# Kernel optimization log

Measured on AMD Instinct MI355X. Metric: run time of the kernel, lower is better.

## Reference

```python
import jax, jax.numpy as jnp
import numpy as np
import math

NUM_HEADS = 16
NUM_KV_HEADS = 4
HEAD_DIM = 128
HIDDEN = 2048
ROPE_BASE = 10000.0


def setup_inputs() -> dict:
    key = jax.random.key(0)
    ks = jax.random.split(key, 6)
    B, S = 1, 4096
    hidden_states = jax.random.normal(ks[0], (B, S, HIDDEN), dtype=jnp.float32)
    attention_mask = jnp.ones((B, S), dtype=jnp.int32)
    position_ids = jnp.broadcast_to(jnp.arange(S, dtype=jnp.int32)[None, :], (B, S))
    sc = 1.0 / math.sqrt(HIDDEN)
    wq = jax.random.normal(ks[1], (HIDDEN, NUM_HEADS * HEAD_DIM), dtype=jnp.float32) * sc
    wk = jax.random.normal(ks[2], (HIDDEN, NUM_KV_HEADS * HEAD_DIM), dtype=jnp.float32) * sc
    wv = jax.random.normal(ks[3], (HIDDEN, NUM_KV_HEADS * HEAD_DIM), dtype=jnp.float32) * sc
    wo = jax.random.normal(ks[4], (NUM_HEADS * HEAD_DIM, HIDDEN), dtype=jnp.float32) * sc
    return {"hidden_states": hidden_states, "attention_mask": attention_mask,
            "position_ids": position_ids, "wq": wq, "wk": wk, "wv": wv, "wo": wo}


def _rotate_half(x):
    x1, x2 = jnp.split(x, 2, axis=-1)
    return jnp.concatenate((-x2, x1), axis=-1)


def _rope_tables(seq_len, dtype):
    inv_freq = 1.0 / (ROPE_BASE ** (jnp.arange(0, HEAD_DIM, 2, dtype=jnp.float32) / HEAD_DIM))
    t = jnp.arange(seq_len, dtype=jnp.float32)
    freqs = jnp.outer(t, inv_freq)                       # [S, hd/2]
    emb = jnp.concatenate((freqs, freqs), axis=-1)       # [S, hd]
    return jnp.cos(emb).astype(dtype), jnp.sin(emb).astype(dtype)


def reference(hidden_states, attention_mask, position_ids, wq, wk, wv, wo):
    B, S, _ = hidden_states.shape
    dtype = hidden_states.dtype
    # projections -> [B, H, S, hd]
    q = (hidden_states @ wq).reshape(B, S, NUM_HEADS, HEAD_DIM).transpose(0, 2, 1, 3)
    k = (hidden_states @ wk).reshape(B, S, NUM_KV_HEADS, HEAD_DIM).transpose(0, 2, 1, 3)
    v = (hidden_states @ wv).reshape(B, S, NUM_KV_HEADS, HEAD_DIM).transpose(0, 2, 1, 3)
    # RoPE
    cos_t, sin_t = _rope_tables(S, dtype)
    cos = cos_t[position_ids][:, None]                   # [B,1,S,hd]
    sin = sin_t[position_ids][:, None]
    q = q * cos + _rotate_half(q) * sin
    k = k * cos + _rotate_half(k) * sin
    # GQA repeat
    n_rep = NUM_HEADS // NUM_KV_HEADS
    k = jnp.repeat(k, n_rep, axis=1)
    v = jnp.repeat(v, n_rep, axis=1)
    # scores + causal mask + padding mask
    scores = jnp.einsum('bhqd,bhkd->bhqk', q, k) / math.sqrt(HEAD_DIM)
    neg = jnp.finfo(scores.dtype).min
    causal = jnp.triu(jnp.full((S, S), neg, dtype=scores.dtype), k=1)
    scores = scores + causal[None, None]
    pad = (1.0 - attention_mask.astype(scores.dtype))[:, None, None, :] * neg
    scores = scores + pad
    attn = jax.nn.softmax(scores.astype(jnp.float32), axis=-1).astype(dtype)
    out = jnp.einsum('bhqk,bhkd->bhqd', attn, v)
    out = out.transpose(0, 2, 1, 3).reshape(B, S, NUM_HEADS * HEAD_DIM)
    return out @ wo
```

## Files before the change

### kernel.cpp

```cpp
#include <hip/hip_runtime.h>
#include <cstdint>
#include <cstddef>

typedef unsigned short ushort_t;
typedef short    bf16x8 __attribute__((ext_vector_type(8)));
typedef float    f32x4  __attribute__((ext_vector_type(4)));
typedef uint4    __attribute__((may_alias)) uint4_a;
typedef ushort4  __attribute__((may_alias)) ushort4_a;
typedef float4   __attribute__((may_alias)) float4_a;
typedef float2   __attribute__((may_alias)) float2_a;
typedef unsigned __attribute__((may_alias)) uint_a;

constexpr int SEQ = 4096, HID = 2048, NHEADS = 16, NKVH = 4, HDIM = 128;
constexpr int QD  = NHEADS * HDIM;
constexpr int KVD = NKVH * HDIM;
constexpr int KVL = 2 * KVD;
constexpr int NPART = 56;

static __device__ __forceinline__ float bf2f(ushort_t u) {
    return __uint_as_float(((unsigned)u) << 16);
}
static __device__ __forceinline__ ushort_t f2bf(float f) {
    unsigned x = __float_as_uint(f);
    unsigned r = x + 0x7FFFu + ((x >> 16) & 1u);
    return (ushort_t)(r >> 16);
}
static __device__ __forceinline__ unsigned pack2(float lo, float hi) {
    return (unsigned)f2bf(lo) | ((unsigned)f2bf(hi) << 16);
}
static __device__ __forceinline__ unsigned cvt_pk(float lo, float hi) {
    unsigned r;
    asm("v_cvt_pk_bf16_f32 %0, %1, %2" : "=v"(r) : "v"(lo), "v"(hi));
    return r;
}

static __device__ __forceinline__ void gld16(const ushort_t* g, ushort_t* l) {
    __builtin_amdgcn_global_load_lds(
        (const __attribute__((address_space(1))) unsigned*)g,
        (__attribute__((address_space(3))) unsigned*)l, 16, 0, 0);
}

__global__ __launch_bounds__(256) void cast_f32_bf16(
    const float* __restrict__ in, ushort_t* __restrict__ out, int n)
{
    int i = (blockIdx.x * 256 + threadIdx.x) * 8;
    if (i >= n) return;
    float4 a = *(const float4_a*)(in + i);
    float4 b = *(const float4_a*)(in + i + 4);
    uint4 o;
    o.x = pack2(a.x, a.y); o.y = pack2(a.z, a.w);
    o.z = pack2(b.x, b.y); o.w = pack2(b.z, b.w);
    *(uint4_a*)(out + i) = o;
}

__global__ __launch_bounds__(256) void transpose_cast(
    const float* __restrict__ W, ushort_t* __restrict__ WT, int K, int N)
{
    __shared__ float tl[32][36];
    const int k0 = blockIdx.x * 32, n0 = blockIdx.y * 32;
    const int t  = threadIdx.x;
    {
        int i = t >> 3, jb = (t & 7) * 4;
        *(float4_a*)&tl[i][jb] = *(const float4_a*)(W + (size_t)(k0 + i) * N + n0 + jb);
    }
    __syncthreads();
    {
        int n = t >> 3, kb = (t & 7) * 4;
        ushort4 o;
        o.x = f2bf(tl[kb + 0][n]); o.y = f2bf(tl[kb + 1][n]);
        o.z = f2bf(tl[kb + 2][n]); o.w = f2bf(tl[kb + 3][n]);
        *(ushort4_a*)(WT + (size_t)(n0 + n) * K + k0 + kb) = o;
    }
}

__global__ __launch_bounds__(256) void gemm_mfma(
    const ushort_t* __restrict__ A, int lda,
    const ushort_t* __restrict__ Bt, int ldb,
    void* __restrict__ C1, int ld1, void* __restrict__ C2, int ld2,
    int split, int N, int K, int out_f32)
{
    __shared__ ushort_t as[128 * 32];
    __shared__ ushort_t bs[128 * 32];

    const int t    = threadIdx.x;
    const int mb   = blockIdx.y * 128, nb = blockIdx.x * 128;
    const int w    = t >> 6, lane = t & 63, quad = lane >> 4, l15 = lane & 15;
    const int wm   = (w >> 1) * 64, wn = (w & 1) * 64;

    const int dr_row = lane >> 2, dr_c = lane & 3;
    const int rA0 = w * 16 + dr_row, rA1 = 64 + w * 16 + dr_row;
    const ushort_t* a0p = A  + (size_t)(mb + rA0) * lda + (dr_c ^ (rA0 & 3)) * 8;
    const ushort_t* a1p = A  + (size_t)(mb + rA1) * lda + (dr_c ^ (rA1 & 3)) * 8;
    const ushort_t* b0p = Bt + (size_t)(nb + rA0) * ldb + (dr_c ^ (rA0 & 3)) * 8;
    const ushort_t* b1p = Bt + (size_t)(nb + rA1) * ldb + (dr_c ^ (rA1 & 3)) * 8;
    ushort_t* asb0 = &as[(w) * 512];        ushort_t* asb1 = &as[(4 + w) * 512];
    ushort_t* bsb0 = &bs[(w) * 512];        ushort_t* bsb1 = &bs[(4 + w) * 512];

    f32x4 acc[4][4];
#pragma unroll
    for (int i = 0; i < 4; i++)
#pragma unroll
        for (int j = 0; j < 4; j++) acc[i][j] = (f32x4)0.f;

    const int chunk = quad ^ (l15 & 3);

    for (int kb = 0; kb < K; kb += 32) {
        __syncthreads();
        gld16(a0p + kb, asb0);
        gld16(a1p + kb, asb1);
        gld16(b0p + kb, bsb0);
        gld16(b1p + kb, bsb1);
        __syncthreads();

        bf16x8 af[4], bf[4];
#pragma unroll
        for (int mt = 0; mt < 4; mt++)
            af[mt] = *(const bf16x8*)&as[(wm + mt * 16 + l15) * 32 + chunk * 8];
#pragma unroll
        for (int nt = 0; nt < 4; nt++)
            bf[nt] = *(const bf16x8*)&bs[(wn + nt * 16 + l15) * 32 + chunk * 8];
#pragma unroll
        for (int mt = 0; mt < 4; mt++)
#pragma unroll
            for (int nt = 0; nt < 4; nt++)
                acc[mt][nt] = __builtin_amdgcn_mfma_f32_16x16x32_bf16(
                    af[mt], bf[nt], acc[mt][nt], 0, 0, 0);
    }

#pragma unroll
    for (int mt = 0; mt < 4; mt++)
#pragma unroll
        for (int nt = 0; nt < 4; nt++) {
            int colg = nb + wn + nt * 16 + l15;
#pragma unroll
            for (int r = 0; r < 4; r++) {
                int row = mb + wm + mt * 16 + quad * 4 + r;
                float v = acc[mt][nt][r];
                if (out_f32)            ((float*)C1)[(size_t)row * ld1 + colg] = v;
                else if (colg < split)  ((ushort_t*)C1)[(size_t)row * ld1 + colg] = f2bf(v);
                else                    ((ushort_t*)C2)[(size_t)row * ld2 + colg - split] = f2bf(v);
            }
        }
}

__global__ __launch_bounds__(256) void rope_bf16(
    ushort_t* __restrict__ buf, int ld, int nh, const int* __restrict__ pos_ids)
{
    int idx  = blockIdx.x * 256 + threadIdx.x;
    int i    = idx & 63;
    int rem  = idx >> 6;
    int head = rem % nh;
    int s    = rem / nh;
    if (s >= SEQ) return;

    float pos = (float)pos_ids[s];
    float ang = pos * __expf(-(float)i * 0.14391156831212787f);
    float c, sn;
    sincosf(ang, &sn, &c);

    ushort_t* p = buf + (size_t)s * ld + head * HDIM;
    float x0 = bf2f(p[i]);
    float x1 = bf2f(p[i + 64]);
    p[i]      = f2bf(x0 * c - x1 * sn);
    p[i + 64] = f2bf(x1 * c + x0 * sn);
}

__global__ __launch_bounds__(512, 4) void flash_mfma(
    const ushort_t* Q, const ushort_t* __restrict__ KV,
    const int* __restrict__ amask, ushort_t* O,
    ushort_t* __restrict__ Opart, float2* __restrict__ ML)
{
    __shared__ ushort_t ks[64][136];
    __shared__ ushort_t vt[128][72];
    __shared__ float    bias[64];

    const int t = threadIdx.x, w = t >> 6, lane = t & 63;
    const int quad = lane >> 4, l15 = lane & 15;
    const int h = blockIdx.x, kvh = h >> 2;
    const int s = blockIdx.y;
    const int kcol = kvh * HDIM, vcol = KVD + kvh * HDIM;
    const float scale2 = 0.08838834764831845f * 1.44269504088896340f;

    int tile, ktb, kte, pid;
    bool multi;
    if (s < 8)       { tile = 15 - s;        ktb = 0; kte = 2 * tile + 2; multi = false; pid = 0; }
    else if (s < 64) {
        int cs = s - 8;
        int c;
        if (cs < 24) { tile = 16 + cs / 3; c = cs - (tile - 16) * 3; }
        else         { int d = cs - 24; tile = 24 + (d >> 2); c = d & 3; }
        int nkt = 2 * tile + 2;
        ktb = c * 16; kte = (ktb + 16 < nkt) ? ktb + 16 : nkt;
        multi = true; pid = h * NPART + cs;
    }
    else             { tile = 7 - (s - 64);  ktb = 0; kte = 2 * tile + 2; multi = false; pid = 0; }

    const int q0  = tile * 128;
    const int q0w = q0 + w * 16;

    const int krow = t >> 3,  kdo = (t & 7) * 16;
    const int vkp  = t & 31,  vdg = t >> 5;

    int bpi[4];
#pragma unroll
    for (int t4 = 0; t4 < 4; t4++)
        bpi[t4] = ((2 * (quad & 1) + (t4 >> 1)) * 16 + l15) * 4;
    const bool hi_half = (quad >> 1) != 0;

    bf16x8 qf[4];
    {
        const ushort_t* qp = Q + (size_t)(q0w + l15) * QD + h * HDIM;
#pragma unroll
        for (int c = 0; c < 4; c++)
            qf[c] = *(const bf16x8*)(qp + c * 32 + quad * 8);
    }

    f32x4 accO[8];
#pragma unroll
    for (int j = 0; j < 8; j++) accO[j] = (f32x4)0.f;
    float m_s = -1e30f, l_s = 0.f;

    uint4 kst[2], va, vb;
    float bst = 0.f;
    auto stage_load = [&](int kt) {
        const int k0 = kt * 64;
        const ushort_t* kp = KV + (size_t)(k0 + krow) * KVL + kcol + kdo;
        kst[0] = *(const uint4_a*)kp;
        kst[1] = *(const uint4_a*)(kp + 8);
        const ushort_t* vp = KV + (size_t)(k0 + 2 * vkp) * KVL + vcol + vdg * 8;
        va = *(const uint4_a*)vp;
        vb = *(const uint4_a*)(vp + KVL);
        if (t < 64) bst = amask[k0 + t] ? 0.f : -1e30f;
    };

    stage_load(ktb);

    for (int kt = ktb; kt < kte; kt++) {
        const int k0 = kt * 64;
        __syncthreads();
        *(uint4_a*)&ks[krow][kdo]     = kst[0];
        *(uint4_a*)&ks[krow][kdo + 8] = kst[1];
        {
            unsigned aw[4] = {va.x, va.y, va.z, va.w};
            unsigned bw[4] = {vb.x, vb.y, vb.z, vb.w};
#pragma unroll
            for (int i = 0; i < 4; i++) {
                *(uint_a*)&vt[vdg * 8 + 2 * i][2 * vkp] =
                    (aw[i] & 0xFFFFu) | (bw[i] << 16);
                *(uint_a*)&vt[vdg * 8 + 2 * i + 1][2 * vkp] =
                    (aw[i] >> 16) | (bw[i] & 0xFFFF0000u);
            }
        }
        if (t < 64) bias[t] = bst;
        __syncthreads();
        if (kt + 1 < kte) stage_load(kt + 1);

        if (k0 > q0w + 15) continue;

        f32x4 sx[4];
#pragma unroll
        for (int mt = 0; mt < 4; mt++) sx[mt] = (f32x4)0.f;
#pragma unroll
        for (int c = 0; c < 4; c++)
#pragma unroll
            for (int mt = 0; mt < 4; mt++) {
                bf16x8 kf = *(const bf16x8*)&ks[mt * 16 + l15][c * 32 + quad * 8];
                sx[mt] = __builtin_amdgcn_mfma_f32_16x16x32_bf16(kf, qf[c], sx[mt], 0, 0, 0);
            }

        const int qg = q0w + l15;
        const bool full = (k0 + 63 <= q0w);
        float p[4][4];
        float mx = -1e30f;
#pragma unroll
        for (int mt = 0; mt < 4; mt++) {
            float4 b4 = *(const float4_a*)&bias[mt * 16 + quad * 4];
            float br[4] = {b4.x, b4.y, b4.z, b4.w};
#pragma unroll
            for (int r = 0; r < 4; r++) {
                float v = fmaf(sx[mt][r], scale2, br[r]);
                if (!full) {
                    int kg = k0 + mt * 16 + quad * 4 + r;
                    v = (kg > qg) ? -1e30f : v;
                }
                p[mt][r] = v;
                mx = fmaxf(mx, v);
            }
        }
        mx = fmaxf(mx, __shfl_xor(mx, 16));
        mx = fmaxf(mx, __shfl_xor(mx, 32));
        const bool renorm = !__all(mx <= m_s + 8.f);
        const float mnew = renorm ? fmaxf(m_s, mx) : m_s;
        float sum = 0.f;
        unsigned wlo[4], whi[4];
#pragma unroll
        for (int mt = 0; mt < 4; mt++) {
            float p0 = exp2f(p[mt][0] - mnew);
            float p1 = exp2f(p[mt][1] - mnew);
            float p2 = exp2f(p[mt][2] - mnew);
            float p3 = exp2f(p[mt][3] - mnew);
            sum += (p0 + p1) + (p2 + p3);
            wlo[mt] = cvt_pk(p0, p1);
            whi[mt] = cvt_pk(p2, p3);
        }
        sum += __shfl_xor(sum, 16);
        sum += __shfl_xor(sum, 32);

        if (renorm) {
            float alpha = exp2f(m_s - mnew);
            l_s *= alpha;
            float a0 = __shfl(alpha, quad * 4 + 0);
            float a1 = __shfl(alpha, quad * 4 + 1);
            float a2 = __shfl(alpha, quad * 4 + 2);
            float a3 = __shfl(alpha, quad * 4 + 3);
#pragma unroll
            for (int j = 0; j < 8; j++) {
                f32x4 a = accO[j];
                a[0] *= a0; a[1] *= a1; a[2] *= a2; a[3] *= a3;
                accO[j] = a;
            }
        }
        m_s = mnew;
        l_s += sum;

#pragma unroll
        for (int kc = 0; kc < 2; kc++) {
            union { unsigned u[4]; bf16x8 v; } pf;
#pragma unroll
            for (int t4 = 0; t4 < 4; t4++) {
                unsigned slo = (t4 & 1) ? whi[2 * kc]     : wlo[2 * kc];
                unsigned shi = (t4 & 1) ? whi[2 * kc + 1] : wlo[2 * kc + 1];
                int ra = __builtin_amdgcn_ds_bpermute(bpi[t4], (int)slo);
                int rb = __builtin_amdgcn_ds_bpermute(bpi[t4], (int)shi);
                pf.u[t4] = (unsigned)(hi_half ? rb : ra);
            }
#pragma unroll
            for (int n8 = 0; n8 < 8; n8++) {
                bf16x8 vf = *(const bf16x8*)&vt[n8 * 16 + l15][kc * 32 + quad * 8];
                accO[n8] = __builtin_amdgcn_mfma_f32_16x16x32_bf16(pf.v, vf, accO[n8], 0, 0, 0);
            }
        }
    }

    if (!multi) {
        float linv = 1.0f / l_s;
#pragma unroll
        for (int r = 0; r < 4; r++) {
            float lr = __shfl(linv, quad * 4 + r);
            int row = q0w + quad * 4 + r;
            ushort_t* op = O + (size_t)row * QD + h * HDIM;
#pragma unroll
            for (int n8 = 0; n8 < 8; n8++)
                op[n8 * 16 + l15] = f2bf(accO[n8][r] * lr);
        }
    } else {
        ushort_t* op = Opart + (size_t)pid * (128 * 128);
#pragma unroll
        for (int r = 0; r < 4; r++) {
            int row = w * 16 + quad * 4 + r;
#pragma unroll
            for (int n8 = 0; n8 < 8; n8++)
                op[row * 128 + n8 * 16 + l15] = f2bf(accO[n8][r]);
        }
        if (quad == 0)
            ML[pid * 128 + w * 16 + l15] = make_float2(m_s, l_s);
    }
}

__global__ __launch_bounds__(256) void combine_partials(
    const ushort_t* __restrict__ P, const float2* __restrict__ ML,
    ushort_t* __restrict__ O)
{
    const int h = blockIdx.x >> 4, tt = blockIdx.x & 15, tile = 16 + tt;
    const int nc = (tile < 24) ? 3 : 4;
    const int pid0 = h * NPART + ((tile < 24) ? tt * 3 : 24 + (tile - 24) * 4);
    const int tid = threadIdx.x;
    const int row = tid >> 1, dh = (tid & 1) << 6;

    float m_[4], l_[4];
    float M = -1e30f;
#pragma unroll
    for (int c = 0; c < 4; c++) {
        if (c < nc) {
            float2 v = *(const float2_a*)&ML[(pid0 + c) * 128 + row];
            m_[c] = v.x; l_[c] = v.y; M = fmaxf(M, v.x);
        } else { m_[c] = -1e30f; l_[c] = 0.f; }
    }
    float L = 0.f, wgt[4];
#pragma unroll
    for (int c = 0; c < 4; c++) { wgt[c] = exp2f(m_[c] - M); L += wgt[c] * l_[c]; }
    const float inv = 1.0f / L;

    ushort_t* op = O + (size_t)(tile * 128 + row) * QD + h * HDIM + dh;
    const size_t pbase = (size_t)row * 128 + dh;
#pragma unroll
    for (int g = 0; g < 8; g++) {
        float acc[8] = {0.f, 0.f, 0.f, 0.f, 0.f, 0.f, 0.f, 0.f};
#pragma unroll
        for (int c = 0; c < 4; c++) {
            if (c < nc) {
                const ushort_t* pp = P + (size_t)(pid0 + c) * (128 * 128) + pbase + g * 8;
                uint4 v = *(const uint4_a*)pp;
                unsigned u[4] = {v.x, v.y, v.z, v.w};
#pragma unroll
                for (int j = 0; j < 4; j++) {
                    acc[2 * j]     += wgt[c] * bf2f((ushort_t)(u[j] & 0xFFFFu));
                    acc[2 * j + 1] += wgt[c] * bf2f((ushort_t)(u[j] >> 16));
                }
            }
        }
        uint4 o;
        o.x = pack2(acc[0] * inv, acc[1] * inv); o.y = pack2(acc[2] * inv, acc[3] * inv);
        o.z = pack2(acc[4] * inv, acc[5] * inv); o.w = pack2(acc[6] * inv, acc[7] * inv);
        *(uint4_a*)(op + g * 8) = o;
    }
}

extern "C" void kernel_launch(void* const* d_in, const int* in_sizes, int n_in,
                              void* d_out, int out_size, void* d_ws, size_t ws_size,
                              hipStream_t stream)
{
    const float* x     = (const float*)d_in[0];
    const int*   amask = (const int*)d_in[1];
    const int*   pos   = (const int*)d_in[2];
    const float* wq    = (const float*)d_in[3];
    const float* wk    = (const float*)d_in[4];
    const float* wv    = (const float*)d_in[5];
    const float* wo    = (const float*)d_in[6];
    float* out = (float*)d_out;

    ushort_t* wqkvT = (ushort_t*)d_out;
    ushort_t* xb    = wqkvT + (size_t)3072 * HID;

    ushort_t* qbuf  = (ushort_t*)d_ws;
    ushort_t* kvbuf = qbuf + (size_t)SEQ * QD;
    ushort_t* woT   = kvbuf;

    ushort_t* opart = (ushort_t*)d_out;
    float2*   mlbuf = (float2*)((char*)d_out + (size_t)16 * NPART * 128 * 128 * 2);

    cast_f32_bf16<<<SEQ * HID / 8 / 256, 256, 0, stream>>>(x, xb, SEQ * HID);
    transpose_cast<<<dim3(HID / 32, QD / 32),  256, 0, stream>>>(wq, wqkvT, HID, QD);
    transpose_cast<<<dim3(HID / 32, KVD / 32), 256, 0, stream>>>(wk, wqkvT + (size_t)QD * HID, HID, KVD);
    transpose_cast<<<dim3(HID / 32, KVD / 32), 256, 0, stream>>>(wv, wqkvT + (size_t)(QD + KVD) * HID, HID, KVD);

    gemm_mfma<<<dim3(3072 / 128, SEQ / 128), 256, 0, stream>>>(
        xb, HID, wqkvT, HID, qbuf, QD, kvbuf, KVL, QD, 3072, HID, 0);

    rope_bf16<<<SEQ * NHEADS * 64 / 256, 256, 0, stream>>>(qbuf, QD, NHEADS, pos);
    rope_bf16<<<SEQ * NKVH  * 64 / 256, 256, 0, stream>>>(kvbuf, KVL, NKVH, pos);

    flash_mfma<<<dim3(NHEADS, 72), 512, 0, stream>>>(
        qbuf, kvbuf, amask, qbuf, opart, mlbuf);
    combine_partials<<<dim3(256), 256, 0, stream>>>(opart, mlbuf, qbuf);

    transpose_cast<<<dim3(QD / 32, HID / 32), 256, 0, stream>>>(wo, woT, QD, HID);
    gemm_mfma<<<dim3(HID / 128, SEQ / 128), 256, 0, stream>>>(
        qbuf, QD, woT, QD, out, HID, out, HID, HID, HID, QD, 1);
}
```

Baseline: 467.4 us.

## Stage 128-key KV tiles per barrier and raise MFMA wave priority

```diff
diff --git a/kernel.cpp b/kernel.cpp
--- a/kernel.cpp
+++ b/kernel.cpp
@@ -170,9 +170,9 @@
     const int* __restrict__ amask, ushort_t* O,
     ushort_t* __restrict__ Opart, float2* __restrict__ ML)
 {
-    __shared__ ushort_t ks[64][136];
-    __shared__ ushort_t vt[128][72];
-    __shared__ float    bias[64];
+    __shared__ ushort_t ks[128][136];
+    __shared__ ushort_t vt[128][136];
+    __shared__ float    bias[128];
 
     const int t = threadIdx.x, w = t >> 6, lane = t & 63;
     const int quad = lane >> 4, l15 = lane & 15;
@@ -198,8 +198,8 @@
     const int q0  = tile * 128;
     const int q0w = q0 + w * 16;
 
-    const int krow = t >> 3,  kdo = (t & 7) * 16;
-    const int vkp  = t & 31,  vdg = t >> 5;
+    const int krow = t >> 2,  kdo = (t & 3) * 32;
+    const int vkp  = t & 63,  vdg = t >> 6;
 
     int bpi[4];
 #pragma unroll
@@ -220,124 +220,148 @@
     for (int j = 0; j < 8; j++) accO[j] = (f32x4)0.f;
     float m_s = -1e30f, l_s = 0.f;
 
-    uint4 kst[2], va, vb;
+    uint4 kst0, kst1, kst2, kst3, va0, va1, vb0, vb1;
     float bst = 0.f;
-    auto stage_load = [&](int kt) {
-        const int k0 = kt * 64;
+    auto stage_load = [&](int st) {
+        const int k0 = st * 128;
         const ushort_t* kp = KV + (size_t)(k0 + krow) * KVL + kcol + kdo;
-        kst[0] = *(const uint4_a*)kp;
-        kst[1] = *(const uint4_a*)(kp + 8);
-        const ushort_t* vp = KV + (size_t)(k0 + 2 * vkp) * KVL + vcol + vdg * 8;
-        va = *(const uint4_a*)vp;
-        vb = *(const uint4_a*)(vp + KVL);
-        if (t < 64) bst = amask[k0 + t] ? 0.f : -1e30f;
+        kst0 = *(const uint4_a*)kp;
+        kst1 = *(const uint4_a*)(kp + 8);
+        kst2 = *(const uint4_a*)(kp + 16);
+        kst3 = *(const uint4_a*)(kp + 24);
+        const ushort_t* vp = KV + (size_t)(k0 + 2 * vkp) * KVL + vcol + vdg * 16;
+        va0 = *(const uint4_a*)vp;
+        va1 = *(const uint4_a*)(vp + 8);
+        vb0 = *(const uint4_a*)(vp + KVL);
+        vb1 = *(const uint4_a*)(vp + KVL + 8);
+        if (t < 128) bst = amask[k0 + t] ? 0.f : -1e30f;
     };
 
-    stage_load(ktb);
-
-    for (int kt = ktb; kt < kte; kt++) {
-        const int k0 = kt * 64;
+    const int stb = ktb >> 1, ste = kte >> 1;
+    stage_load(stb);
+
+    for (int st = stb; st < ste; st++) {
         __syncthreads();
-        *(uint4_a*)&ks[krow][kdo]     = kst[0];
-        *(uint4_a*)&ks[krow][kdo + 8] = kst[1];
+        *(uint4_a*)&ks[krow][kdo]      = kst0;
+        *(uint4_a*)&ks[krow][kdo + 8]  = kst1;
+        *(uint4_a*)&ks[krow][kdo + 16] = kst2;
+        *(uint4_a*)&ks[krow][kdo + 24] = kst3;
         {
-            unsigned aw[4] = {va.x, va.y, va.z, va.w};
-            unsigned bw[4] = {vb.x, vb.y, vb.z, vb.w};
+            unsigned aw[4] = {va0.x, va0.y, va0.z, va0.w};
+            unsigned bw[4] = {vb0.x, vb0.y, vb0.z, vb0.w};
 #pragma unroll
             for (int i = 0; i < 4; i++) {
-                *(uint_a*)&vt[vdg * 8 + 2 * i][2 * vkp] =
+                *(uint_a*)&vt[vdg * 16 + 2 * i][2 * vkp] =
                     (aw[i] & 0xFFFFu) | (bw[i] << 16);
-                *(uint_a*)&vt[vdg * 8 + 2 * i + 1][2 * vkp] =
+                *(uint_a*)&vt[vdg * 16 + 2 * i + 1][2 * vkp] =
                     (aw[i] >> 16) | (bw[i] & 0xFFFF0000u);
             }
-        }
-        if (t < 64) bias[t] = bst;
+            unsigned aw2[4] = {va1.x, va1.y, va1.z, va1.w};
+            unsigned bw2[4] = {vb1.x, vb1.y, vb1.z, vb1.w};
+#pragma unroll
+            for (int i = 0; i < 4; i++) {
+                *(uint_a*)&vt[vdg * 16 + 8 + 2 * i][2 * vkp] =
+                    (aw2[i] & 0xFFFFu) | (bw2[i] << 16);
+                *(uint_a*)&vt[vdg * 16 + 8 + 2 * i + 1][2 * vkp] =
+                    (aw2[i] >> 16) | (bw2[i] & 0xFFFF0000u);
+            }
+        }
+        if (t < 128) bias[t] = bst;
         __syncthreads();
-        if (kt + 1 < kte) stage_load(kt + 1);
-
-        if (k0 > q0w + 15) continue;
-
-        f32x4 sx[4];
-#pragma unroll
-        for (int mt = 0; mt < 4; mt++) sx[mt] = (f32x4)0.f;
-#pragma unroll
-        for (int c = 0; c < 4; c++)
+        if (st + 1 < ste) stage_load(st + 1);
+
+#pragma unroll
+        for (int ss = 0; ss < 2; ss++) {
+            const int k0 = st * 128 + ss * 64;
+            if (k0 > q0w + 15) continue;
+            const int kb = ss * 64;
+
+            f32x4 sx[4];
+#pragma unroll
+            for (int mt = 0; mt < 4; mt++) sx[mt] = (f32x4)0.f;
+            __builtin_amdgcn_s_setprio(1);
+#pragma unroll
+            for (int c = 0; c < 4; c++)
+#pragma unroll
+                for (int mt = 0; mt < 4; mt++) {
+                    bf16x8 kf = *(const bf16x8*)&ks[kb + mt * 16 + l15][c * 32 + quad * 8];
+                    sx[mt] = __builtin_amdgcn_mfma_f32_16x16x32_bf16(kf, qf[c], sx[mt], 0, 0, 0);
+                }
+            __builtin_amdgcn_s_setprio(0);
+
+            const int qg = q0w + l15;
+            const bool full = (k0 + 63 <= q0w);
+            float p[4][4];
+            float mx = -1e30f;
 #pragma unroll
             for (int mt = 0; mt < 4; mt++) {
-                bf16x8 kf = *(const bf16x8*)&ks[mt * 16 + l15][c * 32 + quad * 8];
-                sx[mt] = __builtin_amdgcn_mfma_f32_16x16x32_bf16(kf, qf[c], sx[mt], 0, 0, 0);
-            }
-
-        const int qg = q0w + l15;
-        const bool full = (k0 + 63 <= q0w);
-        float p[4][4];
-        float mx = -1e30f;
-#pragma unroll
-        for (int mt = 0; mt < 4; mt++) {
-            float4 b4 = *(const float4_a*)&bias[mt * 16 + quad * 4];
-            float br[4] = {b4.x, b4.y, b4.z, b4.w};
-#pragma unroll
-            for (int r = 0; r < 4; r++) {
-                float v = fmaf(sx[mt][r], scale2, br[r]);
-                if (!full) {
-                    int kg = k0 + mt * 16 + quad * 4 + r;
-                    v = (kg > qg) ? -1e30f : v;
-                }
-                p[mt][r] = v;
-                mx = fmaxf(mx, v);
-            }
-        }
-        mx = fmaxf(mx, __shfl_xor(mx, 16));
-        mx = fmaxf(mx, __shfl_xor(mx, 32));
-        const bool renorm = !__all(mx <= m_s + 8.f);
-        const float mnew = renorm ? fmaxf(m_s, mx) : m_s;
-        float sum = 0.f;
-        unsigned wlo[4], whi[4];
-#pragma unroll
-        for (int mt = 0; mt < 4; mt++) {
-            float p0 = exp2f(p[mt][0] - mnew);
-            float p1 = exp2f(p[mt][1] - mnew);
-            float p2 = exp2f(p[mt][2] - mnew);
-            float p3 = exp2f(p[mt][3] - mnew);
-            sum += (p0 + p1) + (p2 + p3);
-            wlo[mt] = cvt_pk(p0, p1);
-            whi[mt] = cvt_pk(p2, p3);
-        }
-        sum += __shfl_xor(sum, 16);
-        sum += __shfl_xor(sum, 32);
-
-        if (renorm) {
-            float alpha = exp2f(m_s - mnew);
-            l_s *= alpha;
-            float a0 = __shfl(alpha, quad * 4 + 0);
-            float a1 = __shfl(alpha, quad * 4 + 1);
-            float a2 = __shfl(alpha, quad * 4 + 2);
-            float a3 = __shfl(alpha, quad * 4 + 3);
-#pragma unroll
-            for (int j = 0; j < 8; j++) {
-                f32x4 a = accO[j];
-                a[0] *= a0; a[1] *= a1; a[2] *= a2; a[3] *= a3;
-                accO[j] = a;
-            }
-        }
-        m_s = mnew;
-        l_s += sum;
-
-#pragma unroll
-        for (int kc = 0; kc < 2; kc++) {
-            union { unsigned u[4]; bf16x8 v; } pf;
-#pragma unroll
-            for (int t4 = 0; t4 < 4; t4++) {
-                unsigned slo = (t4 & 1) ? whi[2 * kc]     : wlo[2 * kc];
-                unsigned shi = (t4 & 1) ? whi[2 * kc + 1] : wlo[2 * kc + 1];
-                int ra = __builtin_amdgcn_ds_bpermute(bpi[t4], (int)slo);
-                int rb = __builtin_amdgcn_ds_bpermute(bpi[t4], (int)shi);
-                pf.u[t4] = (unsigned)(hi_half ? rb : ra);
-            }
-#pragma unroll
-            for (int n8 = 0; n8 < 8; n8++) {
-                bf16x8 vf = *(const bf16x8*)&vt[n8 * 16 + l15][kc * 32 + quad * 8];
-                accO[n8] = __builtin_amdgcn_mfma_f32_16x16x32_bf16(pf.v, vf, accO[n8], 0, 0, 0);
+                float4 b4 = *(const float4_a*)&bias[kb + mt * 16 + quad * 4];
+                float br[4] = {b4.x, b4.y, b4.z, b4.w};
+#pragma unroll
+                for (int r = 0; r < 4; r++) {
+                    float v = fmaf(sx[mt][r], scale2, br[r]);
+                    if (!full) {
+                        int kg = k0 + mt * 16 + quad * 4 + r;
+                        v = (kg > qg) ? -1e30f : v;
+                    }
+                    p[mt][r] = v;
+                    mx = fmaxf(mx, v);
+                }
+            }
+            mx = fmaxf(mx, __shfl_xor(mx, 16));
+            mx = fmaxf(mx, __shfl_xor(mx, 32));
+            const bool renorm = !__all(mx <= m_s + 8.f);
+            const float mnew = renorm ? fmaxf(m_s, mx) : m_s;
+            float sum = 0.f;
+            unsigned wlo[4], whi[4];
+#pragma unroll
+            for (int mt = 0; mt < 4; mt++) {
+                float p0 = exp2f(p[mt][0] - mnew);
+                float p1 = exp2f(p[mt][1] - mnew);
+                float p2 = exp2f(p[mt][2] - mnew);
+                float p3 = exp2f(p[mt][3] - mnew);
+                sum += (p0 + p1) + (p2 + p3);
+                wlo[mt] = cvt_pk(p0, p1);
+                whi[mt] = cvt_pk(p2, p3);
+            }
+            sum += __shfl_xor(sum, 16);
+            sum += __shfl_xor(sum, 32);
+
+            if (renorm) {
+                float alpha = exp2f(m_s - mnew);
+                l_s *= alpha;
+                float a0 = __shfl(alpha, quad * 4 + 0);
+                float a1 = __shfl(alpha, quad * 4 + 1);
+                float a2 = __shfl(alpha, quad * 4 + 2);
+                float a3 = __shfl(alpha, quad * 4 + 3);
+#pragma unroll
+                for (int j = 0; j < 8; j++) {
+                    f32x4 a = accO[j];
+                    a[0] *= a0; a[1] *= a1; a[2] *= a2; a[3] *= a3;
+                    accO[j] = a;
+                }
+            }
+            m_s = mnew;
+            l_s += sum;
+
+#pragma unroll
+            for (int kc = 0; kc < 2; kc++) {
+                union { unsigned u[4]; bf16x8 v; } pf;
+#pragma unroll
+                for (int t4 = 0; t4 < 4; t4++) {
+                    unsigned slo = (t4 & 1) ? whi[2 * kc]     : wlo[2 * kc];
+                    unsigned shi = (t4 & 1) ? whi[2 * kc + 1] : wlo[2 * kc + 1];
+                    int ra = __builtin_amdgcn_ds_bpermute(bpi[t4], (int)slo);
+                    int rb = __builtin_amdgcn_ds_bpermute(bpi[t4], (int)shi);
+                    pf.u[t4] = (unsigned)(hi_half ? rb : ra);
+                }
+                __builtin_amdgcn_s_setprio(1);
+#pragma unroll
+                for (int n8 = 0; n8 < 8; n8++) {
+                    bf16x8 vf = *(const bf16x8*)&vt[n8 * 16 + l15][kb + kc * 32 + quad * 8];
+                    accO[n8] = __builtin_amdgcn_mfma_f32_16x16x32_bf16(pf.v, vf, accO[n8], 0, 0, 0);
+                }
+                __builtin_amdgcn_s_setprio(0);
             }
         }
     }
```

Result: slower. 478.1 us (+2.3%).
